# Kernel tuning notes

Measured on AMD Instinct MI355X. Metric: run time of the kernel, lower is better.

The kernel has to match this reference:

```python
import jax, jax.numpy as jnp
import numpy as np

B, S, C, H = 2, 3144, 256, 8
HD = C // H                      # head_dim = key_dim = 32
SCALE = HD ** -0.5
QN = 8                           # queriesNum hard-coded in source
KS = 5                           # lepe depthwise conv kernel


def setup_inputs() -> dict:
    key = jax.random.key(0)
    ks = jax.random.split(key, 10)
    gain_qkv = 2 ** (-2.5) * (2.0 / (C + C)) ** 0.5  # xavier_normal std with gain 2^-2.5
    gain_out = (2.0 / (C + C)) ** 0.5
    return {
        "x": jax.random.normal(ks[0], (B, S, C), jnp.float32),
        "mask": jax.random.uniform(ks[1], (B, S, S), jnp.float32),
        "wq": jax.random.normal(ks[2], (C, C), jnp.float32) * gain_qkv,
        "bq": jnp.zeros((C,), jnp.float32),
        "wk": jax.random.normal(ks[3], (C, C), jnp.float32) * gain_qkv,
        "bk": jnp.zeros((C,), jnp.float32),
        "wv": jax.random.normal(ks[4], (C, C), jnp.float32) * gain_qkv,
        "bv": jnp.zeros((C,), jnp.float32),
        "lepe_w": jax.random.normal(ks[5], (KS, KS, 1, C), jnp.float32) * 0.05,  # depthwise HWIO
        "lepe_b": jnp.zeros((C,), jnp.float32),
        "wo": jax.random.normal(ks[6], (C, C), jnp.float32) * gain_out,
        "bo": jnp.zeros((C,), jnp.float32),
        "h": 56,
        "w": 56,
    }


def _dwconv(x_nhwc, kern, bias):
    # depthwise 5x5, stride 1, padding 2 (groups = channels)
    y = jax.lax.conv_general_dilated(
        x_nhwc, kern, window_strides=(1, 1), padding=((2, 2), (2, 2)),
        dimension_numbers=("NHWC", "HWIO", "NHWC"),
        feature_group_count=x_nhwc.shape[-1])
    return y + bias


def reference(x, mask, wq, bq, wk, bk, wv, bv, lepe_w, lepe_b, wo, bo, h, w):
    b, s, c = x.shape
    q = x @ wq.T + bq
    k = (x @ wk.T + bk) * SCALE
    v = x @ wv.T + bv
    # lepe positional residual on the non-query tokens
    lepe = _dwconv(v[:, QN:].reshape(b, h, w, c), lepe_w, lepe_b).reshape(b, h * w, c)
    qh = q.reshape(b, s, H, HD).transpose(0, 2, 1, 3)   # (b, H, s, hd)
    kh = k.reshape(b, s, H, HD).transpose(0, 2, 1, 3)
    vh = kh  # faithful to source: v_h = k.reshape(...)  (scaled k used as values)
    qk = jnp.einsum("bhqd,bhkd->bhqk", qh, kh)
    qk = qk + jnp.log(mask[:, None] + 1e-6)              # isSoftMask=True path
    attn = jax.nn.softmax(qk, axis=-1)
    out = jnp.einsum("bhqk,bhkd->bhqd", attn, vh)
    out = out.transpose(0, 2, 1, 3).reshape(b, s, c)
    out = out.at[:, QN:].add(lepe)
    return out @ wo.T + bo
```

## Files before the change

kernel.cpp:

```cpp
#include <hip/hip_runtime.h>


#define S_LEN 3144
#define SP    3200
#define HEADS 8
#define HD    32
#define BATCH 2
#define MROWS (BATCH*S_LEN)
#define NPIX  3136
#define SCALE_F 0.17677669529663687f
#define KQ_SC   0.25504472665352026f

typedef __bf16 bf16x8  __attribute__((ext_vector_type(8)));
typedef __bf16 bf16x4  __attribute__((ext_vector_type(4)));
typedef float  floatx4 __attribute__((ext_vector_type(4)));
typedef short  shortx4 __attribute__((ext_vector_type(4)));

static __device__ __forceinline__ float bf2f(unsigned int h) {
  union { unsigned int u; float f; } v; v.u = h << 16; return v.f;
}
static __device__ __forceinline__ unsigned short f2bf(float f) {
  union { __bf16 b; unsigned short u; } v; v.b = (__bf16)f; return v.u;
}
static __device__ __forceinline__ bf16x8 ldcvt8(const float* __restrict__ p) {
  float4 a = *(const float4*)p;
  float4 b = *(const float4*)(p + 4);
  bf16x8 r;
  r[0]=(__bf16)a.x; r[1]=(__bf16)a.y; r[2]=(__bf16)a.z; r[3]=(__bf16)a.w;
  r[4]=(__bf16)b.x; r[5]=(__bf16)b.y; r[6]=(__bf16)b.z; r[7]=(__bf16)b.w;
  return r;
}

#define GLOBAL_AS __attribute__((address_space(1)))
#define LDS_AS    __attribute__((address_space(3)))
static __device__ __forceinline__ void gload_lds16(const void* g, void* l) {
  __builtin_amdgcn_global_load_lds((const GLOBAL_AS void*)g, (LDS_AS void*)l, 16, 0, 0);
}

#define FENCE4() asm volatile("s_waitcnt vmcnt(4)" ::: "memory")
#define FENCE0() asm volatile("s_waitcnt vmcnt(0)" ::: "memory")

__global__ __launch_bounds__(256) void k_cvt(
    const float* __restrict__ x, const float* __restrict__ wq,
    const float* __restrict__ wk, const float* __restrict__ wv,
    unsigned short* __restrict__ xb, unsigned short* __restrict__ w3b)
{
  const int i = blockIdx.x * 256 + threadIdx.x;
  const int NX = MROWS * 32;
  const int NW = 8192;
  const float* src;
  unsigned short* dst;
  if (i < NX) { src = x + (size_t)i * 8; dst = xb + (size_t)i * 8; }
  else {
    const int j = i - NX;
    if (j >= 3 * NW) return;
    src = (j < NW) ? wq + (size_t)j * 8
        : (j < 2 * NW) ? wk + (size_t)(j - NW) * 8
                       : wv + (size_t)(j - 2 * NW) * 8;
    dst = w3b + (size_t)j * 8;
  }
  bf16x8 v = ldcvt8(src);
  *(bf16x8*)dst = v;
}

__global__ __launch_bounds__(256) void k_mprep(const float* __restrict__ mask,
                                               float* __restrict__ pm)
{
  const int bs = blockIdx.x;
  const int b  = bs / 200, strip = bs % 200;
  const int tid = threadIdx.x;
  const int i  = tid >> 6, l = tid & 63;
  const int rq = i * 4 + (l >> 4);
  int mr = strip * 16 + rq; if (mr >= S_LEN) mr = S_LEN - 1;
  const int cg = ((l & 15) ^ rq) & 15;
  const float* src = mask + ((size_t)b * S_LEN + mr) * S_LEN;
  float* dst = pm + (size_t)bs * (50 * 1024) + tid * 4;
#pragma unroll 1
  for (int tt = 0; tt < 10; ++tt) {
    const int t = blockIdx.y * 10 + tt;
    const int c0 = t * 64 + cg * 4;
    float4 o;
    if (c0 < S_LEN) {
      float4 mv = *(const float4*)(src + c0);
      o.x = __log2f(mv.x + 1e-6f);
      o.y = __log2f(mv.y + 1e-6f);
      o.z = __log2f(mv.z + 1e-6f);
      o.w = __log2f(mv.w + 1e-6f);
    } else {
      o = make_float4(-1e30f, -1e30f, -1e30f, -1e30f);
    }
    *(float4*)(dst + (size_t)t * 1024) = o;
  }
}

__global__ __launch_bounds__(256) void k_qkv(
    const unsigned short* __restrict__ xb, const unsigned short* __restrict__ w3b,
    const float* __restrict__ bqp, const float* __restrict__ bkp,
    const float* __restrict__ bvp,
    unsigned short* __restrict__ qws, unsigned short* __restrict__ kws,
    unsigned short* __restrict__ vfrag, unsigned short* __restrict__ vstage)
{
  __shared__ unsigned short lds_t[64 * 65];
  const int lane = threadIdx.x & 63;
  const int wid  = threadIdx.x >> 6;
  const int c    = lane & 15, quad = lane >> 4;
  const int bsel  = blockIdx.x / 50;
  const int stile = blockIdx.x % 50;
  const int srow0 = stile * 64;
  const int ncol = blockIdx.y * 64;
  const int wsel = ncol >> 8;
  const int col0 = ncol & 255;

  const float* bptr = (wsel == 0) ? bqp : (wsel == 1) ? bkp : bvp;

  const int srow = srow0 + wid * 16 + c;
  const int arow = bsel * S_LEN + ((srow < S_LEN) ? srow : 0);
  const unsigned short* ap = xb  + (size_t)arow * 256 + quad * 8;
  const unsigned short* bp = w3b + (size_t)(ncol + c) * 256 + quad * 8;

  floatx4 acc[4];
#pragma unroll
  for (int ct = 0; ct < 4; ++ct) acc[ct] = (floatx4){0.f, 0.f, 0.f, 0.f};

#pragma unroll
  for (int ks = 0; ks < 8; ++ks) {
    bf16x8 af = *(const bf16x8*)(ap + ks * 32);
#pragma unroll
    for (int ct = 0; ct < 4; ++ct) {
      bf16x8 bf = *(const bf16x8*)(bp + (size_t)ct * 16 * 256 + ks * 32);
      acc[ct] = __builtin_amdgcn_mfma_f32_16x16x32_bf16(af, bf, acc[ct], 0, 0, 0);
    }
  }

#pragma unroll
  for (int ct = 0; ct < 4; ++ct) {
    const int col = col0 + ct * 16 + c;
    const float bias = bptr[col];
#pragma unroll
    for (int r = 0; r < 4; ++r) {
      const int s = srow0 + wid * 16 + quad * 4 + r;
      const int valid = (s < S_LEN);
      const float v = acc[ct][r] + bias;
      if (wsel == 0) {
        qws[(((size_t)(bsel * HEADS + (col >> 5))) * SP + s) * HD + (col & 31)] =
            valid ? f2bf(v) : (unsigned short)0;
      } else if (wsel == 1) {
        kws[(((size_t)(bsel * HEADS + (col >> 5))) * SP + s) * HD + (col & 31)] =
            valid ? f2bf(v * KQ_SC) : (unsigned short)0;
        lds_t[(ct * 16 + c) * 65 + (wid * 16 + quad * 4 + r)] =
            valid ? f2bf(v * SCALE_F) : (unsigned short)0;
      } else {
        if (valid) vstage[(size_t)(bsel * S_LEN + s) * 256 + col] = f2bf(v);
      }
    }
  }

  if (wsel == 1) {
    __syncthreads();
    const int tid = threadIdx.x;
#pragma unroll
    for (int j = 0; j < 4; ++j) {
      const int grp  = j * 4 + (tid >> 6);
      const int l    = tid & 63;
      const int ct2  = grp & 3;
      const int half = (grp >> 2) & 1;
      const int hsel = grp >> 3;
      const int cc = l & 15, qq = l >> 4;
      const int cl = hsel * 32 + half * 16 + cc;
      const int rb = ct2 * 16 + qq * 4;
      union { shortx4 s4; unsigned short u[4]; } pk;
#pragma unroll
      for (int e = 0; e < 4; ++e) pk.u[e] = lds_t[cl * 65 + rb + e];
      const int hglob = (col0 >> 5) + hsel;
      const size_t off =
          ((((size_t)(bsel * HEADS + hglob) * 50 + stile) * 4 + ct2) * 2 + half) * 64 + l;
      *(shortx4*)(vfrag + off * 4) = pk.s4;
    }
  }
}

__global__ __launch_bounds__(256) void k_lepe(const unsigned short* __restrict__ vws,
                                              const float* __restrict__ cw,
                                              const float* __restrict__ cb,
                                              unsigned short* __restrict__ lepe)
{
  int idx = blockIdx.x * 256 + threadIdx.x;
  if (idx >= BATCH * NPIX * 32) return;
  const int cg = idx & 31;
  const int p  = (idx >> 5) % NPIX;
  const int b  = idx / (NPIX * 32);
  const int y  = p / 56, xx = p - y * 56;

  float acc[8];
  {
    float4 b0 = *(const float4*)(cb + cg * 8);
    float4 b1 = *(const float4*)(cb + cg * 8 + 4);
    acc[0]=b0.x; acc[1]=b0.y; acc[2]=b0.z; acc[3]=b0.w;
    acc[4]=b1.x; acc[5]=b1.y; acc[6]=b1.z; acc[7]=b1.w;
  }
#pragma unroll
  for (int dy = -2; dy <= 2; ++dy) {
    const int yy = y + dy;
    if ((unsigned)yy >= 56u) continue;
#pragma unroll
    for (int dx = -2; dx <= 2; ++dx) {
      const int xs = xx + dx;
      if ((unsigned)xs >= 56u) continue;
      uint4 vv = *(const uint4*)(vws + (size_t)(b * S_LEN + 8 + yy * 56 + xs) * 256 + cg * 8);
      const float* wp = cw + (size_t)((dy + 2) * 5 + (dx + 2)) * 256 + cg * 8;
      float4 w0 = *(const float4*)wp;
      float4 w1 = *(const float4*)(wp + 4);
      unsigned int va[4] = {vv.x, vv.y, vv.z, vv.w};
      acc[0] += bf2f(va[0] & 0xFFFFu) * w0.x;  acc[1] += bf2f(va[0] >> 16) * w0.y;
      acc[2] += bf2f(va[1] & 0xFFFFu) * w0.z;  acc[3] += bf2f(va[1] >> 16) * w0.w;
      acc[4] += bf2f(va[2] & 0xFFFFu) * w1.x;  acc[5] += bf2f(va[2] >> 16) * w1.y;
      acc[6] += bf2f(va[3] & 0xFFFFu) * w1.z;  acc[7] += bf2f(va[3] >> 16) * w1.w;
    }
  }
  unsigned int o[4];
#pragma unroll
  for (int j = 0; j < 4; ++j)
    o[j] = (unsigned int)f2bf(acc[2*j]) | ((unsigned int)f2bf(acc[2*j+1]) << 16);
  *((uint4*)(lepe + (size_t)(b * NPIX + p) * 256 + cg * 8)) = make_uint4(o[0], o[1], o[2], o[3]);
}

static __device__ __forceinline__ void proc_tile_pre(
    int t, const unsigned short* __restrict__ kb,
    const unsigned short* __restrict__ vb,
    const float* __restrict__ mb,
    int c, int quad, int lane, const bf16x8 qf,
    floatx4& o0, floatx4& o1, float& l_run)
{
  const int k0 = t * 64;
  bf16x8 kf[4]; shortx4 v0[4], v1[4];
  const unsigned short* tb = vb + (size_t)t * 2048;
#pragma unroll
  for (int ct = 0; ct < 4; ++ct) {
    kf[ct] = *(const bf16x8*)(kb + (size_t)(k0 + ct * 16 + c) * HD + quad * 8);
    v0[ct] = *(const shortx4*)(tb + (ct * 2 + 0) * 256 + lane * 4);
    v1[ct] = *(const shortx4*)(tb + (ct * 2 + 1) * 256 + lane * 4);
  }
  floatx4 s[4];
#pragma unroll
  for (int ct = 0; ct < 4; ++ct)
    s[ct] = __builtin_amdgcn_mfma_f32_16x16x32_bf16(kf[ct], qf,
               (floatx4){0.f,0.f,0.f,0.f}, 0, 0, 0);
  float ls = 0.f;
  shortx4 pf[4];
#pragma unroll
  for (int ct = 0; ct < 4; ++ct) {
    const float4 mv = *(const float4*)(mb + c * 64 + (((ct * 4 + quad) ^ c) * 4));
    float pr[4];
    pr[0] = __builtin_amdgcn_exp2f(s[ct][0] + mv.x);
    pr[1] = __builtin_amdgcn_exp2f(s[ct][1] + mv.y);
    pr[2] = __builtin_amdgcn_exp2f(s[ct][2] + mv.z);
    pr[3] = __builtin_amdgcn_exp2f(s[ct][3] + mv.w);
    ls += (pr[0] + pr[1]) + (pr[2] + pr[3]);
    union { bf16x4 b4; shortx4 s4; } u;
    u.b4[0]=(__bf16)pr[0]; u.b4[1]=(__bf16)pr[1]; u.b4[2]=(__bf16)pr[2]; u.b4[3]=(__bf16)pr[3];
    pf[ct] = u.s4;
  }
  l_run += ls;
#pragma unroll
  for (int ct = 0; ct < 4; ++ct) {
    o0 = __builtin_amdgcn_mfma_f32_16x16x16bf16_1k(v0[ct], pf[ct], o0, 0, 0, 0);
    o1 = __builtin_amdgcn_mfma_f32_16x16x16bf16_1k(v1[ct], pf[ct], o1, 0, 0, 0);
  }
}

static __device__ __forceinline__ void stage_pre(
    const float* __restrict__ mp_t, int lane, float* dst)
{
#pragma unroll
  for (int i = 0; i < 4; ++i)
    gload_lds16(mp_t + i * 256 + lane * 4, dst + i * 256);
}

__global__ __launch_bounds__(512) void k_flash_pre(
    const unsigned short* __restrict__ qws,
    const unsigned short* __restrict__ kws,
    const unsigned short* __restrict__ vfrag,
    const float* __restrict__ pmask,
    const unsigned short* __restrict__ lepe,
    unsigned short* __restrict__ attn)
{
  __shared__ __align__(16) float smem[8][2048];
  const int lane = threadIdx.x & 63;
  const int wid  = threadIdx.x >> 6;
  const int c    = lane & 15, quad = lane >> 4;
  const int u    = blockIdx.x;
  const int xcd  = u & 7;
  const int slot = u >> 3;
  const int h    = slot & 7;
  const int p    = (slot >> 3) * 8 + xcd;
  const int b    = p / 200;
  const int strip = p - b * 200;
  const int qrow = strip * 16 + c;
  const size_t bh = (size_t)(b * HEADS + h);

  const bf16x8 qf = *(const bf16x8*)(qws + (bh * SP + qrow) * HD + quad * 8);
  const unsigned short* kb = kws + bh * SP * HD;
  const unsigned short* vb = vfrag + bh * (size_t)(50 * 2048);
  const float* mpb = pmask + (size_t)(b * 200 + strip) * (50 * 1024);
  float* mt = &smem[wid][0];

  float l_run = 0.f;
  floatx4 o0 = (floatx4){0.f,0.f,0.f,0.f};
  floatx4 o1 = (floatx4){0.f,0.f,0.f,0.f};

  const int tbase = wid * 6;
  const int nt = (wid < 2) ? 7 : 6;

  stage_pre(mpb + tbase * 1024, lane, mt);

  for (int it = 0; it < nt; ++it) {
    const int t = (it < 6) ? tbase + it : 48 + wid;
    if (it + 1 < nt) {
      const int tn = (it + 1 < 6) ? tbase + it + 1 : 48 + wid;
      stage_pre(mpb + tn * 1024, lane, mt + ((it + 1) & 1) * 1024);
      FENCE4();
    } else {
      FENCE0();
    }
    proc_tile_pre(t, kb, vb, mt + (it & 1) * 1024, c, quad, lane, qf, o0, o1, l_run);
  }

#pragma unroll
  for (int r = 0; r < 4; ++r) {
    smem[wid][lane * 9 + r]     = o0[r];
    smem[wid][lane * 9 + 4 + r] = o1[r];
  }
  smem[wid][lane * 9 + 8] = l_run;
  __syncthreads();

  if (wid == 0) {
#pragma unroll
    for (int w = 1; w < 8; ++w) {
#pragma unroll
      for (int r = 0; r < 4; ++r) {
        o0[r] += smem[w][lane * 9 + r];
        o1[r] += smem[w][lane * 9 + 4 + r];
      }
      l_run += smem[w][lane * 9 + 8];
    }
    l_run += __shfl_xor(l_run, 16);
    l_run += __shfl_xor(l_run, 32);
    const float rl = 1.f / l_run;

    if (qrow < S_LEN) {
      const size_t obase = ((size_t)b * S_LEN + qrow) * 256 + h * 32;
      const size_t lbase = (qrow >= 8) ? (((size_t)b * NPIX + (qrow - 8)) * 256 + h * 32) : 0;
#pragma unroll
      for (int mt2 = 0; mt2 < 2; ++mt2) {
        floatx4 ov = mt2 ? o1 : o0;
#pragma unroll
        for (int r = 0; r < 4; ++r) {
          const int d = mt2 * 16 + quad * 4 + r;
          float val = ov[r] * rl;
          if (qrow >= 8) val += bf2f(lepe[lbase + d]);
          attn[obase + d] = f2bf(val);
        }
      }
    }
  }
}

template<bool TAIL>
static __device__ __forceinline__ void proc_tile_fb(
    int t, const unsigned short* __restrict__ kb,
    const unsigned short* __restrict__ vb,
    const float* __restrict__ mb,
    int c, int quad, int lane, const bf16x8 qf,
    floatx4& o0, floatx4& o1, float& l_run)
{
  const int k0 = t * 64;
  bf16x8 kf[4]; shortx4 v0[4], v1[4];
  const unsigned short* tb = vb + (size_t)t * 2048;
#pragma unroll
  for (int ct = 0; ct < 4; ++ct) {
    kf[ct] = *(const bf16x8*)(kb + (size_t)(k0 + ct * 16 + c) * HD + quad * 8);
    v0[ct] = *(const shortx4*)(tb + (ct * 2 + 0) * 256 + lane * 4);
    v1[ct] = *(const shortx4*)(tb + (ct * 2 + 1) * 256 + lane * 4);
  }
  floatx4 s[4];
#pragma unroll
  for (int ct = 0; ct < 4; ++ct)
    s[ct] = __builtin_amdgcn_mfma_f32_16x16x32_bf16(kf[ct], qf,
               (floatx4){0.f,0.f,0.f,0.f}, 0, 0, 0);
  float ls = 0.f;
  shortx4 pf[4];
#pragma unroll
  for (int ct = 0; ct < 4; ++ct) {
    const float4 mv = *(const float4*)(mb + c * 64 + (((ct * 4 + quad) ^ c) * 4));
    float pr[4];
    pr[0] = (mv.x + 1e-6f) * __builtin_amdgcn_exp2f(s[ct][0]);
    pr[1] = (mv.y + 1e-6f) * __builtin_amdgcn_exp2f(s[ct][1]);
    pr[2] = (mv.z + 1e-6f) * __builtin_amdgcn_exp2f(s[ct][2]);
    pr[3] = (mv.w + 1e-6f) * __builtin_amdgcn_exp2f(s[ct][3]);
    if (TAIL) {
      const int kk = k0 + ct * 16 + quad * 4;
#pragma unroll
      for (int r = 0; r < 4; ++r) if (kk + r >= S_LEN) pr[r] = 0.f;
    }
    ls += (pr[0] + pr[1]) + (pr[2] + pr[3]);
    union { bf16x4 b4; shortx4 s4; } u;
    u.b4[0]=(__bf16)pr[0]; u.b4[1]=(__bf16)pr[1]; u.b4[2]=(__bf16)pr[2]; u.b4[3]=(__bf16)pr[3];
    pf[ct] = u.s4;
  }
  l_run += ls;
#pragma unroll
  for (int ct = 0; ct < 4; ++ct) {
    o0 = __builtin_amdgcn_mfma_f32_16x16x16bf16_1k(v0[ct], pf[ct], o0, 0, 0, 0);
    o1 = __builtin_amdgcn_mfma_f32_16x16x16bf16_1k(v1[ct], pf[ct], o1, 0, 0, 0);
  }
}

static __device__ __forceinline__ void stage_mask_fb(
    const float* const (&msrc)[4], const int (&goff4)[4], int k0, float* dst)
{
#pragma unroll
  for (int i = 0; i < 4; ++i)
    gload_lds16(msrc[i] + (k0 + goff4[i]), dst + i * 256);
}

static __device__ __forceinline__ void stage_mask_tail_fb(
    const float* const (&msrc)[4], const int (&goff4)[4], int k0, float* dst)
{
#pragma unroll
  for (int i = 0; i < 4; ++i) {
    int kk = k0 + goff4[i];
    if (kk > S_LEN - 4) kk = S_LEN - 4;
    gload_lds16(msrc[i] + kk, dst + i * 256);
  }
}

__global__ __launch_bounds__(512) void k_flash_fb(
    const unsigned short* __restrict__ qws,
    const unsigned short* __restrict__ kws,
    const unsigned short* __restrict__ vfrag,
    const float* __restrict__ mask,
    const unsigned short* __restrict__ lepe,
    unsigned short* __restrict__ attn)
{
  __shared__ __align__(16) float smem[8][2048];
  const int lane = threadIdx.x & 63;
  const int wid  = threadIdx.x >> 6;
  const int c    = lane & 15, quad = lane >> 4;
  const int u    = blockIdx.x;
  const int xcd  = u & 7;
  const int slot = u >> 3;
  const int h    = slot & 7;
  const int p    = (slot >> 3) * 8 + xcd;
  const int b    = p / 200;
  const int strip = p - b * 200;
  const int qrow = strip * 16 + c;
  const size_t bh = (size_t)(b * HEADS + h);

  const bf16x8 qf = *(const bf16x8*)(qws + (bh * SP + qrow) * HD + quad * 8);
  const unsigned short* kb = kws + bh * SP * HD;
  const unsigned short* vb = vfrag + bh * (size_t)(50 * 2048);
  float* mt = &smem[wid][0];

  const float* msrc[4];
  int goff4[4];
#pragma unroll
  for (int i = 0; i < 4; ++i) {
    const int rq = i * 4 + (lane >> 4);
    int mr = strip * 16 + rq; if (mr >= S_LEN) mr = S_LEN - 1;
    msrc[i] = mask + ((size_t)b * S_LEN + mr) * S_LEN;
    goff4[i] = ((lane & 15) ^ rq) * 4;
  }

  float l_run = 0.f;
  floatx4 o0 = (floatx4){0.f,0.f,0.f,0.f};
  floatx4 o1 = (floatx4){0.f,0.f,0.f,0.f};

  const int tbase = wid * 6;
  const int nt = (wid < 2) ? 7 : 6;

  stage_mask_fb(msrc, goff4, tbase * 64, mt);

  for (int it = 0; it < nt; ++it) {
    const int t = (it < 6) ? tbase + it : 48 + wid;
    if (it + 1 < nt) {
      const int tn = (it + 1 < 6) ? tbase + it + 1 : 48 + wid;
      float* dst = mt + ((it + 1) & 1) * 1024;
      if (tn == 49) stage_mask_tail_fb(msrc, goff4, 49 * 64, dst);
      else          stage_mask_fb(msrc, goff4, tn * 64, dst);
      FENCE4();
    } else {
      FENCE0();
    }
    const float* mb = mt + (it & 1) * 1024;
    if (wid == 1 && it == 6)
      proc_tile_fb<true >(t, kb, vb, mb, c, quad, lane, qf, o0, o1, l_run);
    else
      proc_tile_fb<false>(t, kb, vb, mb, c, quad, lane, qf, o0, o1, l_run);
  }

#pragma unroll
  for (int r = 0; r < 4; ++r) {
    smem[wid][lane * 9 + r]     = o0[r];
    smem[wid][lane * 9 + 4 + r] = o1[r];
  }
  smem[wid][lane * 9 + 8] = l_run;
  __syncthreads();

  if (wid == 0) {
#pragma unroll
    for (int w = 1; w < 8; ++w) {
#pragma unroll
      for (int r = 0; r < 4; ++r) {
        o0[r] += smem[w][lane * 9 + r];
        o1[r] += smem[w][lane * 9 + 4 + r];
      }
      l_run += smem[w][lane * 9 + 8];
    }
    l_run += __shfl_xor(l_run, 16);
    l_run += __shfl_xor(l_run, 32);
    const float rl = 1.f / l_run;

    if (qrow < S_LEN) {
      const size_t obase = ((size_t)b * S_LEN + qrow) * 256 + h * 32;
      const size_t lbase = (qrow >= 8) ? (((size_t)b * NPIX + (qrow - 8)) * 256 + h * 32) : 0;
#pragma unroll
      for (int mt2 = 0; mt2 < 2; ++mt2) {
        floatx4 ov = mt2 ? o1 : o0;
#pragma unroll
        for (int r = 0; r < 4; ++r) {
          const int d = mt2 * 16 + quad * 4 + r;
          float val = ov[r] * rl;
          if (qrow >= 8) val += bf2f(lepe[lbase + d]);
          attn[obase + d] = f2bf(val);
        }
      }
    }
  }
}

__global__ __launch_bounds__(256) void k_oproj(
    const unsigned short* __restrict__ attn,
    const float* __restrict__ wop,
    const float* __restrict__ bop,
    float* __restrict__ out)
{
  const int lane = threadIdx.x & 63;
  const int wid  = threadIdx.x >> 6;
  const int c = lane & 15, quad = lane >> 4;
  const int row0 = blockIdx.x * 64 + wid * 16;
  const int col0 = blockIdx.y * 64;

  int arow = row0 + c; if (arow >= MROWS) arow = 0;
  const unsigned short* ap = attn + (size_t)arow * 256 + quad * 8;
  const float* bp = wop + (size_t)(col0 + c) * 256 + quad * 8;

  floatx4 acc[4];
#pragma unroll
  for (int ct = 0; ct < 4; ++ct) acc[ct] = (floatx4){0.f,0.f,0.f,0.f};
#pragma unroll
  for (int ks = 0; ks < 8; ++ks) {
    bf16x8 af = *(const bf16x8*)(ap + ks * 32);
#pragma unroll
    for (int ct = 0; ct < 4; ++ct) {
      bf16x8 bf = ldcvt8(bp + (size_t)ct * 16 * 256 + ks * 32);
      acc[ct] = __builtin_amdgcn_mfma_f32_16x16x32_bf16(af, bf, acc[ct], 0, 0, 0);
    }
  }
#pragma unroll
  for (int ct = 0; ct < 4; ++ct) {
    const int col = col0 + ct * 16 + c;
    const float bias = bop[col];
#pragma unroll
    for (int r = 0; r < 4; ++r) {
      const int row = row0 + quad * 4 + r;
      if (row >= MROWS) continue;
      out[(size_t)row * 256 + col] = acc[ct][r] + bias;
    }
  }
}

#define QW_OFF 0u
#define KW_OFF 3276800u
#define VF_OFF 6553600u
#define LE_OFF 9830400u
#define AT_OFF 13041664u
#define PM_OFF 16261120u
#define PM_NEED (16261120u + 81920000u)

extern "C" void kernel_launch(void* const* d_in, const int* in_sizes, int n_in,
                              void* d_out, int out_size, void* d_ws, size_t ws_size,
                              hipStream_t stream) {
  const float* x    = (const float*)d_in[0];
  const float* mask = (const float*)d_in[1];
  const float* wq   = (const float*)d_in[2];
  const float* bq   = (const float*)d_in[3];
  const float* wk   = (const float*)d_in[4];
  const float* bk   = (const float*)d_in[5];
  const float* wv   = (const float*)d_in[6];
  const float* bv   = (const float*)d_in[7];
  const float* lw   = (const float*)d_in[8];
  const float* lb   = (const float*)d_in[9];
  const float* wo   = (const float*)d_in[10];
  const float* bo   = (const float*)d_in[11];

  char* ws = (char*)d_ws;
  unsigned short* qws = (unsigned short*)(ws + QW_OFF);
  unsigned short* kws = (unsigned short*)(ws + KW_OFF);
  unsigned short* vfr = (unsigned short*)(ws + VF_OFF);
  unsigned short* w3b = (unsigned short*)(ws + LE_OFF);
  unsigned short* lpe = (unsigned short*)(ws + LE_OFF);
  unsigned short* atb = (unsigned short*)(ws + AT_OFF);
  unsigned short* vst = (unsigned short*)d_out;
  unsigned short* xb  = (unsigned short*)d_out + 1609728;
  float*          outf = (float*)d_out;

  const bool use_pre = (ws_size >= (size_t)PM_NEED);

  k_cvt<<<882, 256, 0, stream>>>(x, wq, wk, wv, xb, w3b);
  if (use_pre) {
    float* pm = (float*)(ws + PM_OFF);
    k_mprep<<<dim3(400, 5), 256, 0, stream>>>(mask, pm);
    k_qkv<<<dim3(100, 12), 256, 0, stream>>>(xb, w3b, bq, bk, bv, qws, kws, vfr, vst);
    k_lepe<<<784, 256, 0, stream>>>(vst, lw, lb, lpe);
    k_flash_pre<<<3200, 512, 0, stream>>>(qws, kws, vfr, pm, lpe, atb);
  } else {
    k_qkv<<<dim3(100, 12), 256, 0, stream>>>(xb, w3b, bq, bk, bv, qws, kws, vfr, vst);
    k_lepe<<<784, 256, 0, stream>>>(vst, lw, lb, lpe);
    k_flash_fb<<<3200, 512, 0, stream>>>(qws, kws, vfr, mask, lpe, atb);
  }
  k_oproj<<<dim3(99, 4), 256, 0, stream>>>(atb, wo, bo, outf);
}
```

Baseline: 326.7 us.

## Store preprocessed mask as fp16 linear values and multiply after exp2

```diff
diff --git a/kernel.cpp b/kernel.cpp
--- a/kernel.cpp
+++ b/kernel.cpp
@@ -15,6 +15,8 @@
 typedef __bf16 bf16x4  __attribute__((ext_vector_type(4)));
 typedef float  floatx4 __attribute__((ext_vector_type(4)));
 typedef short  shortx4 __attribute__((ext_vector_type(4)));
+typedef _Float16 halfx4 __attribute__((ext_vector_type(4)));
+typedef _Float16 halfx8 __attribute__((ext_vector_type(8)));
 
 static __device__ __forceinline__ float bf2f(unsigned int h) {
   union { unsigned int u; float f; } v; v.u = h << 16; return v.f;
@@ -38,6 +40,7 @@
 }
 
 #define FENCE4() asm volatile("s_waitcnt vmcnt(4)" ::: "memory")
+#define FENCE2() asm volatile("s_waitcnt vmcnt(2)" ::: "memory")
 #define FENCE0() asm volatile("s_waitcnt vmcnt(0)" ::: "memory")
 
 __global__ __launch_bounds__(256) void k_cvt(
@@ -64,32 +67,41 @@
 }
 
 __global__ __launch_bounds__(256) void k_mprep(const float* __restrict__ mask,
-                                               float* __restrict__ pm)
+                                               _Float16* __restrict__ pm)
 {
   const int bs = blockIdx.x;
   const int b  = bs / 200, strip = bs % 200;
-  const int tid = threadIdx.x;
-  const int i  = tid >> 6, l = tid & 63;
-  const int rq = i * 4 + (l >> 4);
-  int mr = strip * 16 + rq; if (mr >= S_LEN) mr = S_LEN - 1;
-  const int cg = ((l & 15) ^ rq) & 15;
+  const int t  = threadIdx.x;
+  const int n  = t & 127;
+  const int tsel = t >> 7;
+  const int row = n >> 3;
+  const int k2  = n & 7;
+  const int g0  = (2 * k2) ^ (row & 15);
+  const int gbase = g0 & ~1;
+  const bool swp = (g0 & 1);
+
+  int mr = strip * 16 + row; if (mr >= S_LEN) mr = S_LEN - 1;
   const float* src = mask + ((size_t)b * S_LEN + mr) * S_LEN;
-  float* dst = pm + (size_t)bs * (50 * 1024) + tid * 4;
+  _Float16* dst0 = pm + ((size_t)bs * 50) * 1024 + n * 8;
+
 #pragma unroll 1
-  for (int tt = 0; tt < 10; ++tt) {
-    const int t = blockIdx.y * 10 + tt;
-    const int c0 = t * 64 + cg * 4;
-    float4 o;
+  for (int tt = 0; tt < 5; ++tt) {
+    const int tile = blockIdx.y * 10 + tt * 2 + tsel;
+    const int c0 = tile * 64 + gbase * 4;
+    float4 a = make_float4(-1e-6f, -1e-6f, -1e-6f, -1e-6f);
+    float4 c = a;
     if (c0 < S_LEN) {
-      float4 mv = *(const float4*)(src + c0);
-      o.x = __log2f(mv.x + 1e-6f);
-      o.y = __log2f(mv.y + 1e-6f);
-      o.z = __log2f(mv.z + 1e-6f);
-      o.w = __log2f(mv.w + 1e-6f);
-    } else {
-      o = make_float4(-1e30f, -1e30f, -1e30f, -1e30f);
-    }
-    *(float4*)(dst + (size_t)t * 1024) = o;
+      a = *(const float4*)(src + c0);
+      c = *(const float4*)(src + c0 + 4);
+    }
+    const float4 fst = swp ? c : a;
+    const float4 snd = swp ? a : c;
+    halfx8 o;
+    o[0] = (_Float16)(fst.x + 1e-6f); o[1] = (_Float16)(fst.y + 1e-6f);
+    o[2] = (_Float16)(fst.z + 1e-6f); o[3] = (_Float16)(fst.w + 1e-6f);
+    o[4] = (_Float16)(snd.x + 1e-6f); o[5] = (_Float16)(snd.y + 1e-6f);
+    o[6] = (_Float16)(snd.z + 1e-6f); o[7] = (_Float16)(snd.w + 1e-6f);
+    *(halfx8*)(dst0 + (size_t)tile * 1024) = o;
   }
 }
 
@@ -227,7 +239,7 @@
 static __device__ __forceinline__ void proc_tile_pre(
     int t, const unsigned short* __restrict__ kb,
     const unsigned short* __restrict__ vb,
-    const float* __restrict__ mb,
+    const _Float16* __restrict__ mb,
     int c, int quad, int lane, const bf16x8 qf,
     floatx4& o0, floatx4& o1, float& l_run)
 {
@@ -249,12 +261,12 @@
   shortx4 pf[4];
 #pragma unroll
   for (int ct = 0; ct < 4; ++ct) {
-    const float4 mv = *(const float4*)(mb + c * 64 + (((ct * 4 + quad) ^ c) * 4));
+    const halfx4 mv = *(const halfx4*)(mb + c * 64 + (((ct * 4 + quad) ^ c) * 4));
     float pr[4];
-    pr[0] = __builtin_amdgcn_exp2f(s[ct][0] + mv.x);
-    pr[1] = __builtin_amdgcn_exp2f(s[ct][1] + mv.y);
-    pr[2] = __builtin_amdgcn_exp2f(s[ct][2] + mv.z);
-    pr[3] = __builtin_amdgcn_exp2f(s[ct][3] + mv.w);
+    pr[0] = (float)mv[0] * __builtin_amdgcn_exp2f(s[ct][0]);
+    pr[1] = (float)mv[1] * __builtin_amdgcn_exp2f(s[ct][1]);
+    pr[2] = (float)mv[2] * __builtin_amdgcn_exp2f(s[ct][2]);
+    pr[3] = (float)mv[3] * __builtin_amdgcn_exp2f(s[ct][3]);
     ls += (pr[0] + pr[1]) + (pr[2] + pr[3]);
     union { bf16x4 b4; shortx4 s4; } u;
     u.b4[0]=(__bf16)pr[0]; u.b4[1]=(__bf16)pr[1]; u.b4[2]=(__bf16)pr[2]; u.b4[3]=(__bf16)pr[3];
@@ -269,18 +281,176 @@
 }
 
 static __device__ __forceinline__ void stage_pre(
-    const float* __restrict__ mp_t, int lane, float* dst)
-{
-#pragma unroll
-  for (int i = 0; i < 4; ++i)
-    gload_lds16(mp_t + i * 256 + lane * 4, dst + i * 256);
+    const _Float16* __restrict__ mp_t, int lane, _Float16* dst)
+{
+#pragma unroll
+  for (int i = 0; i < 2; ++i)
+    gload_lds16(mp_t + i * 512 + lane * 8, dst + i * 512);
 }
 
 __global__ __launch_bounds__(512) void k_flash_pre(
     const unsigned short* __restrict__ qws,
     const unsigned short* __restrict__ kws,
     const unsigned short* __restrict__ vfrag,
-    const float* __restrict__ pmask,
+    const _Float16* __restrict__ pmask,
+    const unsigned short* __restrict__ lepe,
+    unsigned short* __restrict__ attn)
+{
+  __shared__ __align__(16) float smem[8][1024];
+  const int lane = threadIdx.x & 63;
+  const int wid  = threadIdx.x >> 6;
+  const int c    = lane & 15, quad = lane >> 4;
+  const int u    = blockIdx.x;
+  const int xcd  = u & 7;
+  const int slot = u >> 3;
+  const int h    = slot & 7;
+  const int p    = (slot >> 3) * 8 + xcd;
+  const int b    = p / 200;
+  const int strip = p - b * 200;
+  const int qrow = strip * 16 + c;
+  const size_t bh = (size_t)(b * HEADS + h);
+
+  const bf16x8 qf = *(const bf16x8*)(qws + (bh * SP + qrow) * HD + quad * 8);
+  const unsigned short* kb = kws + bh * SP * HD;
+  const unsigned short* vb = vfrag + bh * (size_t)(50 * 2048);
+  const _Float16* mpb = pmask + (size_t)(b * 200 + strip) * (50 * 1024);
+  _Float16* mt = (_Float16*)&smem[wid][0];
+
+  float l_run = 0.f;
+  floatx4 o0 = (floatx4){0.f,0.f,0.f,0.f};
+  floatx4 o1 = (floatx4){0.f,0.f,0.f,0.f};
+
+  const int tbase = wid * 6;
+  const int nt = (wid < 2) ? 7 : 6;
+
+  stage_pre(mpb + tbase * 1024, lane, mt);
+
+  for (int it = 0; it < nt; ++it) {
+    const int t = (it < 6) ? tbase + it : 48 + wid;
+    if (it + 1 < nt) {
+      const int tn = (it + 1 < 6) ? tbase + it + 1 : 48 + wid;
+      stage_pre(mpb + tn * 1024, lane, mt + ((it + 1) & 1) * 1024);
+      FENCE2();
+    } else {
+      FENCE0();
+    }
+    proc_tile_pre(t, kb, vb, mt + (it & 1) * 1024, c, quad, lane, qf, o0, o1, l_run);
+  }
+
+#pragma unroll
+  for (int r = 0; r < 4; ++r) {
+    smem[wid][lane * 9 + r]     = o0[r];
+    smem[wid][lane * 9 + 4 + r] = o1[r];
+  }
+  smem[wid][lane * 9 + 8] = l_run;
+  __syncthreads();
+
+  if (wid == 0) {
+#pragma unroll
+    for (int w = 1; w < 8; ++w) {
+#pragma unroll
+      for (int r = 0; r < 4; ++r) {
+        o0[r] += smem[w][lane * 9 + r];
+        o1[r] += smem[w][lane * 9 + 4 + r];
+      }
+      l_run += smem[w][lane * 9 + 8];
+    }
+    l_run += __shfl_xor(l_run, 16);
+    l_run += __shfl_xor(l_run, 32);
+    const float rl = 1.f / l_run;
+
+    if (qrow < S_LEN) {
+      const size_t obase = ((size_t)b * S_LEN + qrow) * 256 + h * 32;
+      const size_t lbase = (qrow >= 8) ? (((size_t)b * NPIX + (qrow - 8)) * 256 + h * 32) : 0;
+#pragma unroll
+      for (int mt2 = 0; mt2 < 2; ++mt2) {
+        floatx4 ov = mt2 ? o1 : o0;
+#pragma unroll
+        for (int r = 0; r < 4; ++r) {
+          const int d = mt2 * 16 + quad * 4 + r;
+          float val = ov[r] * rl;
+          if (qrow >= 8) val += bf2f(lepe[lbase + d]);
+          attn[obase + d] = f2bf(val);
+        }
+      }
+    }
+  }
+}
+
+template<bool TAIL>
+static __device__ __forceinline__ void proc_tile_fb(
+    int t, const unsigned short* __restrict__ kb,
+    const unsigned short* __restrict__ vb,
+    const float* __restrict__ mb,
+    int c, int quad, int lane, const bf16x8 qf,
+    floatx4& o0, floatx4& o1, float& l_run)
+{
+  const int k0 = t * 64;
+  bf16x8 kf[4]; shortx4 v0[4], v1[4];
+  const unsigned short* tb = vb + (size_t)t * 2048;
+#pragma unroll
+  for (int ct = 0; ct < 4; ++ct) {
+    kf[ct] = *(const bf16x8*)(kb + (size_t)(k0 + ct * 16 + c) * HD + quad * 8);
+    v0[ct] = *(const shortx4*)(tb + (ct * 2 + 0) * 256 + lane * 4);
+    v1[ct] = *(const shortx4*)(tb + (ct * 2 + 1) * 256 + lane * 4);
+  }
+  floatx4 s[4];
+#pragma unroll
+  for (int ct = 0; ct < 4; ++ct)
+    s[ct] = __builtin_amdgcn_mfma_f32_16x16x32_bf16(kf[ct], qf,
+               (floatx4){0.f,0.f,0.f,0.f}, 0, 0, 0);
+  float ls = 0.f;
+  shortx4 pf[4];
+#pragma unroll
+  for (int ct = 0; ct < 4; ++ct) {
+    const float4 mv = *(const float4*)(mb + c * 64 + (((ct * 4 + quad) ^ c) * 4));
+    float pr[4];
+    pr[0] = (mv.x + 1e-6f) * __builtin_amdgcn_exp2f(s[ct][0]);
+    pr[1] = (mv.y + 1e-6f) * __builtin_amdgcn_exp2f(s[ct][1]);
+    pr[2] = (mv.z + 1e-6f) * __builtin_amdgcn_exp2f(s[ct][2]);
+    pr[3] = (mv.w + 1e-6f) * __builtin_amdgcn_exp2f(s[ct][3]);
+    if (TAIL) {
+      const int kk = k0 + ct * 16 + quad * 4;
+#pragma unroll
+      for (int r = 0; r < 4; ++r) if (kk + r >= S_LEN) pr[r] = 0.f;
+    }
+    ls += (pr[0] + pr[1]) + (pr[2] + pr[3]);
+    union { bf16x4 b4; shortx4 s4; } u;
+    u.b4[0]=(__bf16)pr[0]; u.b4[1]=(__bf16)pr[1]; u.b4[2]=(__bf16)pr[2]; u.b4[3]=(__bf16)pr[3];
+    pf[ct] = u.s4;
+  }
+  l_run += ls;
+#pragma unroll
+  for (int ct = 0; ct < 4; ++ct) {
+    o0 = __builtin_amdgcn_mfma_f32_16x16x16bf16_1k(v0[ct], pf[ct], o0, 0, 0, 0);
+    o1 = __builtin_amdgcn_mfma_f32_16x16x16bf16_1k(v1[ct], pf[ct], o1, 0, 0, 0);
+  }
+}
+
+static __device__ __forceinline__ void stage_mask_fb(
+    const float* const (&msrc)[4], const int (&goff4)[4], int k0, float* dst)
+{
+#pragma unroll
+  for (int i = 0; i < 4; ++i)
+    gload_lds16(msrc[i] + (k0 + goff4[i]), dst + i * 256);
+}
+
+static __device__ __forceinline__ void stage_mask_tail_fb(
+    const float* const (&msrc)[4], const int (&goff4)[4], int k0, float* dst)
+{
+#pragma unroll
+  for (int i = 0; i < 4; ++i) {
+    int kk = k0 + goff4[i];
+    if (kk > S_LEN - 4) kk = S_LEN - 4;
+    gload_lds16(msrc[i] + kk, dst + i * 256);
+  }
+}
+
+__global__ __launch_bounds__(512) void k_flash_fb(
+    const unsigned short* __restrict__ qws,
+    const unsigned short* __restrict__ kws,
+    const unsigned short* __restrict__ vfrag,
+    const float* __restrict__ mask,
     const unsigned short* __restrict__ lepe,
     unsigned short* __restrict__ attn)
 {
@@ -301,164 +471,6 @@
   const bf16x8 qf = *(const bf16x8*)(qws + (bh * SP + qrow) * HD + quad * 8);
   const unsigned short* kb = kws + bh * SP * HD;
   const unsigned short* vb = vfrag + bh * (size_t)(50 * 2048);
-  const float* mpb = pmask + (size_t)(b * 200 + strip) * (50 * 1024);
-  float* mt = &smem[wid][0];
-
-  float l_run = 0.f;
-  floatx4 o0 = (floatx4){0.f,0.f,0.f,0.f};
-  floatx4 o1 = (floatx4){0.f,0.f,0.f,0.f};
-
-  const int tbase = wid * 6;
-  const int nt = (wid < 2) ? 7 : 6;
-
-  stage_pre(mpb + tbase * 1024, lane, mt);
-
-  for (int it = 0; it < nt; ++it) {
-    const int t = (it < 6) ? tbase + it : 48 + wid;
-    if (it + 1 < nt) {
-      const int tn = (it + 1 < 6) ? tbase + it + 1 : 48 + wid;
-      stage_pre(mpb + tn * 1024, lane, mt + ((it + 1) & 1) * 1024);
-      FENCE4();
-    } else {
-      FENCE0();
-    }
-    proc_tile_pre(t, kb, vb, mt + (it & 1) * 1024, c, quad, lane, qf, o0, o1, l_run);
-  }
-
-#pragma unroll
-  for (int r = 0; r < 4; ++r) {
-    smem[wid][lane * 9 + r]     = o0[r];
-    smem[wid][lane * 9 + 4 + r] = o1[r];
-  }
-  smem[wid][lane * 9 + 8] = l_run;
-  __syncthreads();
-
-  if (wid == 0) {
-#pragma unroll
-    for (int w = 1; w < 8; ++w) {
-#pragma unroll
-      for (int r = 0; r < 4; ++r) {
-        o0[r] += smem[w][lane * 9 + r];
-        o1[r] += smem[w][lane * 9 + 4 + r];
-      }
-      l_run += smem[w][lane * 9 + 8];
-    }
-    l_run += __shfl_xor(l_run, 16);
-    l_run += __shfl_xor(l_run, 32);
-    const float rl = 1.f / l_run;
-
-    if (qrow < S_LEN) {
-      const size_t obase = ((size_t)b * S_LEN + qrow) * 256 + h * 32;
-      const size_t lbase = (qrow >= 8) ? (((size_t)b * NPIX + (qrow - 8)) * 256 + h * 32) : 0;
-#pragma unroll
-      for (int mt2 = 0; mt2 < 2; ++mt2) {
-        floatx4 ov = mt2 ? o1 : o0;
-#pragma unroll
-        for (int r = 0; r < 4; ++r) {
-          const int d = mt2 * 16 + quad * 4 + r;
-          float val = ov[r] * rl;
-          if (qrow >= 8) val += bf2f(lepe[lbase + d]);
-          attn[obase + d] = f2bf(val);
-        }
-      }
-    }
-  }
-}
-
-template<bool TAIL>
-static __device__ __forceinline__ void proc_tile_fb(
-    int t, const unsigned short* __restrict__ kb,
-    const unsigned short* __restrict__ vb,
-    const float* __restrict__ mb,
-    int c, int quad, int lane, const bf16x8 qf,
-    floatx4& o0, floatx4& o1, float& l_run)
-{
-  const int k0 = t * 64;
-  bf16x8 kf[4]; shortx4 v0[4], v1[4];
-  const unsigned short* tb = vb + (size_t)t * 2048;
-#pragma unroll
-  for (int ct = 0; ct < 4; ++ct) {
-    kf[ct] = *(const bf16x8*)(kb + (size_t)(k0 + ct * 16 + c) * HD + quad * 8);
-    v0[ct] = *(const shortx4*)(tb + (ct * 2 + 0) * 256 + lane * 4);
-    v1[ct] = *(const shortx4*)(tb + (ct * 2 + 1) * 256 + lane * 4);
-  }
-  floatx4 s[4];
-#pragma unroll
-  for (int ct = 0; ct < 4; ++ct)
-    s[ct] = __builtin_amdgcn_mfma_f32_16x16x32_bf16(kf[ct], qf,
-               (floatx4){0.f,0.f,0.f,0.f}, 0, 0, 0);
-  float ls = 0.f;
-  shortx4 pf[4];
-#pragma unroll
-  for (int ct = 0; ct < 4; ++ct) {
-    const float4 mv = *(const float4*)(mb + c * 64 + (((ct * 4 + quad) ^ c) * 4));
-    float pr[4];
-    pr[0] = (mv.x + 1e-6f) * __builtin_amdgcn_exp2f(s[ct][0]);
-    pr[1] = (mv.y + 1e-6f) * __builtin_amdgcn_exp2f(s[ct][1]);
-    pr[2] = (mv.z + 1e-6f) * __builtin_amdgcn_exp2f(s[ct][2]);
-    pr[3] = (mv.w + 1e-6f) * __builtin_amdgcn_exp2f(s[ct][3]);
-    if (TAIL) {
-      const int kk = k0 + ct * 16 + quad * 4;
-#pragma unroll
-      for (int r = 0; r < 4; ++r) if (kk + r >= S_LEN) pr[r] = 0.f;
-    }
-    ls += (pr[0] + pr[1]) + (pr[2] + pr[3]);
-    union { bf16x4 b4; shortx4 s4; } u;
-    u.b4[0]=(__bf16)pr[0]; u.b4[1]=(__bf16)pr[1]; u.b4[2]=(__bf16)pr[2]; u.b4[3]=(__bf16)pr[3];
-    pf[ct] = u.s4;
-  }
-  l_run += ls;
-#pragma unroll
-  for (int ct = 0; ct < 4; ++ct) {
-    o0 = __builtin_amdgcn_mfma_f32_16x16x16bf16_1k(v0[ct], pf[ct], o0, 0, 0, 0);
-    o1 = __builtin_amdgcn_mfma_f32_16x16x16bf16_1k(v1[ct], pf[ct], o1, 0, 0, 0);
-  }
-}
-
-static __device__ __forceinline__ void stage_mask_fb(
-    const float* const (&msrc)[4], const int (&goff4)[4], int k0, float* dst)
-{
-#pragma unroll
-  for (int i = 0; i < 4; ++i)
-    gload_lds16(msrc[i] + (k0 + goff4[i]), dst + i * 256);
-}
-
-static __device__ __forceinline__ void stage_mask_tail_fb(
-    const float* const (&msrc)[4], const int (&goff4)[4], int k0, float* dst)
-{
-#pragma unroll
-  for (int i = 0; i < 4; ++i) {
-    int kk = k0 + goff4[i];
-    if (kk > S_LEN - 4) kk = S_LEN - 4;
-    gload_lds16(msrc[i] + kk, dst + i * 256);
-  }
-}
-
-__global__ __launch_bounds__(512) void k_flash_fb(
-    const unsigned short* __restrict__ qws,
-    const unsigned short* __restrict__ kws,
-    const unsigned short* __restrict__ vfrag,
-    const float* __restrict__ mask,
-    const unsigned short* __restrict__ lepe,
-    unsigned short* __restrict__ attn)
-{
-  __shared__ __align__(16) float smem[8][2048];
-  const int lane = threadIdx.x & 63;
-  const int wid  = threadIdx.x >> 6;
-  const int c    = lane & 15, quad = lane >> 4;
-  const int u    = blockIdx.x;
-  const int xcd  = u & 7;
-  const int slot = u >> 3;
-  const int h    = slot & 7;
-  const int p    = (slot >> 3) * 8 + xcd;
-  const int b    = p / 200;
-  const int strip = p - b * 200;
-  const int qrow = strip * 16 + c;
-  const size_t bh = (size_t)(b * HEADS + h);
-
-  const bf16x8 qf = *(const bf16x8*)(qws + (bh * SP + qrow) * HD + quad * 8);
-  const unsigned short* kb = kws + bh * SP * HD;
-  const unsigned short* vb = vfrag + bh * (size_t)(50 * 2048);
   float* mt = &smem[wid][0];
 
   const float* msrc[4];
@@ -585,7 +597,7 @@
 #define LE_OFF 9830400u
 #define AT_OFF 13041664u
 #define PM_OFF 16261120u
-#define PM_NEED (16261120u + 81920000u)
+#define PM_NEED (16261120u + 40960000u)
 
 extern "C" void kernel_launch(void* const* d_in, const int* in_sizes, int n_in,
                               void* d_out, int out_size, void* d_ws, size_t ws_size,
@@ -618,7 +630,7 @@
 
   k_cvt<<<882, 256, 0, stream>>>(x, wq, wk, wv, xb, w3b);
   if (use_pre) {
-    float* pm = (float*)(ws + PM_OFF);
+    _Float16* pm = (_Float16*)(ws + PM_OFF);
     k_mprep<<<dim3(400, 5), 256, 0, stream>>>(mask, pm);
     k_qkv<<<dim3(100, 12), 256, 0, stream>>>(xb, w3b, bq, bk, bv, qws, kws, vfr, vst);
     k_lepe<<<784, 256, 0, stream>>>(vst, lw, lb, lpe);
```

Result: faster. 312.2 us (-4.4%).
